# Performance work log

Measured on AMD Instinct MI355X. Metric: run time of the kernel, lower is better.

The kernel has to match this reference:

```python
import jax, jax.numpy as jnp
import numpy as np

B, C, H, W = 8, 256, 64, 64
HEADS, HID = 8, 64
TMP = HEADS * HID  # 512


def setup_inputs() -> dict:
    key = jax.random.key(0)
    ks = jax.random.split(key, 6)
    s = lambda fan: 1.0 / np.sqrt(fan)
    fmap = jax.random.normal(ks[0], (B, C, H, W), jnp.float32)
    Wq = jax.random.normal(ks[1], (TMP, C), jnp.float32) * s(C)          # to_q 1x1 conv (no bias)
    Wdw = jax.random.normal(ks[2], (C, 1, 3, 3), jnp.float32) * s(9)     # depthwise 3x3 (groups=C, no bias)
    Wkv = jax.random.normal(ks[3], (2 * TMP, C), jnp.float32) * s(C)     # 1x1 conv producing k,v (no bias)
    Wout = jax.random.normal(ks[4], (C, TMP), jnp.float32) * s(TMP)      # to_out 1x1 conv
    bout = jax.random.normal(ks[5], (C,), jnp.float32) * 0.01
    return {"fmap": fmap, "Wq": Wq, "Wdw": Wdw, "Wkv": Wkv, "Wout": Wout, "bout": bout}


def reference(fmap, Wq, Wdw, Wkv, Wout, bout):
    heads, hid = HEADS, HID
    scale = hid ** (-0.5)
    b, c, h, w = fmap.shape
    n = h * w

    # 1x1 conv == channel GEMM
    q = jnp.einsum('bcxy,oc->boxy', fmap, Wq)
    # depthwise 3x3, padding=1
    dw = jax.lax.conv_general_dilated(
        fmap, Wdw, window_strides=(1, 1), padding='SAME',
        dimension_numbers=('NCHW', 'OIHW', 'NCHW'), feature_group_count=c)
    kv = jnp.einsum('bcxy,oc->boxy', dw, Wkv)
    k, v = jnp.split(kv, 2, axis=1)

    # 'b (h c) x y -> b h (x y) c'
    def to_seq(t):
        return t.reshape(b, heads, hid, n).transpose(0, 1, 3, 2)  # [b, h, n, d]

    q, k, v = to_seq(q), to_seq(k), to_seq(v)
    q = jax.nn.softmax(q, axis=-1) * scale   # softmax over feature dim
    k = jax.nn.softmax(k, axis=-2)           # softmax over token dim

    ctx = jnp.einsum('bhnd,bhne->bhde', k, v)    # [b, h, d, d]
    out = jnp.einsum('bhnd,bhde->bhne', q, ctx)  # [b, h, n, d]

    # '(b h) (x y) d -> b (h d) x y'
    out = out.transpose(0, 1, 3, 2).reshape(b, heads * hid, h, w)

    # to_out: GELU (exact) then 1x1 conv with bias (mode='ac')
    out = jax.nn.gelu(out, approximate=False)
    return jnp.einsum('bcxy,oc->boxy', out, Wout) + bout[None, :, None, None]
```

## Files before the change

kernel.cpp:

```cpp
#include <hip/hip_runtime.h>
#include <hip/hip_bf16.h>
#include <math.h>

#define Bx 8
#define Cc 256
#define Nn 4096
#define TMPc 512

typedef unsigned short ushort;
typedef unsigned int uint;
typedef __attribute__((ext_vector_type(8))) short bf16x8;
typedef __attribute__((ext_vector_type(4))) float f32x4;

union F4 { float4 v; float f[4]; };

__device__ __forceinline__ float gelu_exact(float x) {
  return x * 0.5f * (1.0f + erff(x * 0.70710678118654752f));
}
__device__ __forceinline__ ushort f2bf(float x) {
  uint u = __float_as_uint(x);
  uint r = (u + 0x7fffu + ((u >> 16) & 1u)) >> 16;
  return (ushort)r;
}

typedef const __attribute__((address_space(1))) uint* gp1_t;
typedef __attribute__((address_space(3))) uint* lp3_t;
__device__ __forceinline__ void gload16(void* lds, const void* g) {
  __builtin_amdgcn_global_load_lds((gp1_t)g, (lp3_t)lds, 16, 0, 0);
}
__device__ __forceinline__ bf16x8 fragread(const char* lds, int row, int kc) {
  return *(const bf16x8*)(lds + row * 64 + ((kc ^ (row & 3)) << 4));
}

#define CGRP 32
__global__ __launch_bounds__(256) void convfuse_k(const float* __restrict__ fmap,
                                                  const float* __restrict__ Wdw,
                                                  ushort* __restrict__ fmapT,
                                                  ushort* __restrict__ dwT) {
  __shared__ float sin_[CGRP][6 * 64 + 1];
  __shared__ float wl[CGRP][9];
  int t = threadIdx.x;
  int y0 = blockIdx.x * 4;
  int c0 = blockIdx.y * CGRP;
  int z = blockIdx.z;
  for (int i = t; i < CGRP * 9; i += 256) wl[i / 9][i % 9] = Wdw[c0 * 9 + i];
  const float* src = fmap + ((size_t)z * Cc + c0) * 4096;
#pragma unroll
  for (int it = 0; it < 12; ++it) {
    int idx = it * 256 + t;
    int c = idx / 96, rem = idx % 96, yy = rem >> 4, x4 = rem & 15;
    int gy = y0 - 1 + yy;
    F4 v;
    if ((unsigned)gy < 64u)
      v.v = *(const float4*)&src[(size_t)c * 4096 + gy * 64 + x4 * 4];
    else
      v.f[0] = v.f[1] = v.f[2] = v.f[3] = 0.f;
#pragma unroll
    for (int j = 0; j < 4; ++j) sin_[c][yy * 64 + x4 * 4 + j] = v.f[j];
  }
  __syncthreads();
  int c8 = (t & 3) * 8;
  int nl = t >> 2;
  size_t nbase = (size_t)z * 4096 + (size_t)y0 * 64;
#pragma unroll
  for (int it = 0; it < 4; ++it) {
    int n = it * 64 + nl;
    int y = n >> 6, x = n & 63;
    union { ushort u[8]; uint4 q; } fo, go;
#pragma unroll
    for (int cc = 0; cc < 8; ++cc) {
      int c = c8 + cc;
      fo.u[cc] = f2bf(sin_[c][(y + 1) * 64 + x]);
      float acc = 0.f;
#pragma unroll
      for (int dy = 0; dy < 3; ++dy) {
#pragma unroll
        for (int dx = 0; dx < 3; ++dx) {
          int xx = x + dx - 1;
          float pv = ((unsigned)xx < 64u) ? sin_[c][(y + dy) * 64 + xx] : 0.f;
          acc += pv * wl[c][dy * 3 + dx];
        }
      }
      go.u[cc] = f2bf(acc);
    }
    *(uint4*)&fmapT[(nbase + n) * Cc + c0 + c8] = fo.q;
    *(uint4*)&dwT[(nbase + n) * Cc + c0 + c8] = go.q;
  }
}

__global__ __launch_bounds__(256) void cvtb3_k(const float* __restrict__ Wq,
                                               const float* __restrict__ Wkv,
                                               const float* __restrict__ Wout,
                                               ushort* __restrict__ WqB,
                                               ushort* __restrict__ WkvB,
                                               ushort* __restrict__ WoutB) {
  int i = blockIdx.x * 256 + threadIdx.x;
  const float* s;
  ushort* d;
  int idx;
  if (i < 32768) { s = Wq; d = WqB; idx = i; }
  else if (i < 98304) { s = Wkv; d = WkvB; idx = i - 32768; }
  else { s = Wout; d = WoutB; idx = i - 98304; }
  F4 v; v.v = *(const float4*)&s[(size_t)idx * 4];
  union { ushort u[4]; uint2 q; } o;
#pragma unroll
  for (int j = 0; j < 4; ++j) o.u[j] = f2bf(v.f[j]);
  *(uint2*)&d[(size_t)idx * 4] = o.q;
}

__global__ __launch_bounds__(256) void kvgemm_k(const ushort* __restrict__ P,
                                                const ushort* __restrict__ Q,
                                                ushort* __restrict__ Y,
                                                long qz, long yz) {
  __shared__ __align__(16) char lds[16384];
  char* LP = lds;
  char* LQ = lds + 8192;
  int t = threadIdx.x, w = t >> 6, l = t & 63;
  int z = blockIdx.z;
  const ushort* Pz = P + (size_t)(blockIdx.y * 128) * 256;
  const ushort* Qz = Q + (size_t)z * qz + (size_t)(blockIdx.x * 128) * 256;
  f32x4 acc[4][4];
#pragma unroll
  for (int i = 0; i < 4; ++i)
#pragma unroll
    for (int j = 0; j < 4; ++j) acc[i][j] = (f32x4){0.f, 0.f, 0.f, 0.f};
  int wr = (w >> 1) * 64, wc = (w & 1) * 64;
  int rl = l & 15, kc = l >> 4;
  int srow = (l >> 2) & 15, scol = l & 3;

  for (int k0 = 0; k0 < 256; k0 += 32) {
    __syncthreads();
#pragma unroll
    for (int j = 0; j < 2; ++j) {
      int row = (w * 2 + j) * 16 + srow;
      int g = scol ^ (row & 3);
      int off = __builtin_amdgcn_readfirstlane((w * 2 + j) * 1024);
      gload16(LP + off, Pz + (size_t)row * 256 + k0 + g * 8);
      gload16(LQ + off, Qz + (size_t)row * 256 + k0 + g * 8);
    }
    asm volatile("s_waitcnt vmcnt(0)" ::: "memory");
    __syncthreads();
    bf16x8 a[4], b[4];
#pragma unroll
    for (int i = 0; i < 4; ++i) a[i] = fragread(LP, wr + i * 16 + rl, kc);
#pragma unroll
    for (int i = 0; i < 4; ++i) b[i] = fragread(LQ, wc + i * 16 + rl, kc);
#pragma unroll
    for (int i = 0; i < 4; ++i)
#pragma unroll
      for (int j = 0; j < 4; ++j)
        acc[i][j] = __builtin_amdgcn_mfma_f32_16x16x32_bf16(a[i], b[j], acc[i][j], 0, 0, 0);
  }
  int r0 = blockIdx.y * 128 + wr, c0 = blockIdx.x * 128 + wc;
  ushort* Yz = Y + (size_t)z * yz;
#pragma unroll
  for (int i = 0; i < 4; ++i) {
#pragma unroll
    for (int reg = 0; reg < 4; ++reg) {
      int r = r0 + i * 16 + kc * 4 + reg;
#pragma unroll
      for (int j = 0; j < 4; ++j) {
        int c = c0 + j * 16 + rl;
        float v = acc[i][j][reg];
        Yz[(size_t)r * 4096 + c] = f2bf(r < 512 ? __expf(v) : v);
      }
    }
  }
}

__global__ __launch_bounds__(256) void ctx_mfma(const ushort* __restrict__ kv,
                                                float* __restrict__ ctxf,
                                                float* __restrict__ sf) {
  __shared__ __align__(16) char lds[8192];
  int t = threadIdx.x, w = t >> 6, l = t & 63;
  int s = blockIdx.x;
  int h = blockIdx.y & 7, z = blockIdx.y >> 3;
  const ushort* kb = kv + ((size_t)z * 1024 + h * 64) * 4096;
  const ushort* vb = kv + ((size_t)z * 1024 + 512 + h * 64) * 4096;
  f32x4 acc[2][2];
  f32x4 accs[2];
#pragma unroll
  for (int i = 0; i < 2; ++i) {
    accs[i] = (f32x4){0.f, 0.f, 0.f, 0.f};
#pragma unroll
    for (int j = 0; j < 2; ++j) acc[i][j] = (f32x4){0.f, 0.f, 0.f, 0.f};
  }
  bf16x8 ones;
#pragma unroll
  for (int i = 0; i < 8; ++i) ones[i] = (short)0x3F80;
  int wr = (w >> 1) * 32, wc = (w & 1) * 32;
  int rl = l & 15, kc = l >> 4;
  int srow = (l >> 2) & 15, scol = l & 3;
  for (int it = 0; it < 32; ++it) {
    int k0 = s * 1024 + it * 32;
    __syncthreads();
    {
      int row = w * 16 + srow;
      int g = scol ^ (row & 3);
      int off = __builtin_amdgcn_readfirstlane(w * 1024);
      gload16(lds + off, vb + (size_t)row * 4096 + k0 + g * 8);
      gload16(lds + 4096 + off, kb + (size_t)row * 4096 + k0 + g * 8);
    }
    asm volatile("s_waitcnt vmcnt(0)" ::: "memory");
    __syncthreads();
    bf16x8 a[2], b[2];
#pragma unroll
    for (int i = 0; i < 2; ++i) a[i] = fragread(lds, wr + i * 16 + rl, kc);
#pragma unroll
    for (int i = 0; i < 2; ++i) b[i] = fragread(lds + 4096, wc + i * 16 + rl, kc);
#pragma unroll
    for (int i = 0; i < 2; ++i)
#pragma unroll
      for (int j = 0; j < 2; ++j)
        acc[i][j] = __builtin_amdgcn_mfma_f32_16x16x32_bf16(a[i], b[j], acc[i][j], 0, 0, 0);
    if (w < 2) {
#pragma unroll
      for (int j = 0; j < 2; ++j)
        accs[j] = __builtin_amdgcn_mfma_f32_16x16x32_bf16(b[j], ones, accs[j], 0, 0, 0);
    }
  }
  float* cf = ctxf + (size_t)(z * 8 + h) * 4096;
#pragma unroll
  for (int i = 0; i < 2; ++i)
#pragma unroll
    for (int reg = 0; reg < 4; ++reg) {
      int e = wr + i * 16 + kc * 4 + reg;
#pragma unroll
      for (int j = 0; j < 2; ++j) {
        int d = wc + j * 16 + rl;
        atomicAdd(&cf[e * 64 + d], acc[i][j][reg]);
      }
    }
  if (w < 2 && rl == 0) {
    float* sp = sf + (size_t)(z * 8 + h) * 64;
#pragma unroll
    for (int j = 0; j < 2; ++j)
#pragma unroll
      for (int reg = 0; reg < 4; ++reg)
        atomicAdd(&sp[wc + j * 16 + kc * 4 + reg], accs[j][reg]);
  }
}

__global__ __launch_bounds__(256) void ctx_cvt(const float* __restrict__ ctxf,
                                               const float* __restrict__ sf,
                                               ushort* __restrict__ cswz) {
  int page = blockIdx.x;
  const float* s = ctxf + (size_t)page * 4096;
  const float* sp = sf + (size_t)page * 64;
  char* d = (char*)(cswz + (size_t)page * 4096);
  int t = threadIdx.x;
  int e = t >> 2, d0 = (t & 3) * 16;
#pragma unroll
  for (int j = 0; j < 16; ++j) {
    int dd = d0 + j;
    int byte = e * 128 + (((dd >> 3) ^ (e & 7)) << 4) + (dd & 7) * 2;
    *(ushort*)(d + byte) = f2bf(s[e * 64 + dd] / sp[dd]);
  }
}

__global__ __launch_bounds__(256, 2) void qao_k(const ushort* __restrict__ fmapT,
                                                const ushort* __restrict__ WqB,
                                                const ushort* __restrict__ cswz,
                                                const ushort* __restrict__ WoutB,
                                                const float* __restrict__ bout,
                                                float* __restrict__ out) {
  __shared__ __align__(16) char lds[65536];
  char* qbuf = lds;
  char* Bres = lds + 16384;
  char* Asg  = lds + 49152;
  int t = threadIdx.x, w = t >> 6, l = t & 63;
  int z = blockIdx.y, n0 = blockIdx.x * 64;
  int rl = l & 15, kc = l >> 4;
  int srow = (l >> 2) & 15, scol = l & 3;
  int wrd = (w >> 1) * 64;
  int wcn = (w & 1) * 32;
  int hh = w >> 1;

  const ushort* fT = fmapT + ((size_t)z * 4096 + n0) * 256;

#pragma unroll
  for (int p = 0; p < 8; ++p) {
    int row = (w * 8 + p) * 2 + (l >> 5);
    int cs = l & 31;
    int off = __builtin_amdgcn_readfirstlane((w * 8 + p) * 1024);
    gload16(Bres + off, fT + (size_t)row * 256 + ((cs ^ (row & 7)) * 8));
  }

  f32x4 oacc[4][4];
#pragma unroll
  for (int i = 0; i < 4; ++i)
#pragma unroll
    for (int j = 0; j < 4; ++j) oacc[i][j] = (f32x4){0.f, 0.f, 0.f, 0.f};

  asm volatile("s_waitcnt vmcnt(0)" ::: "memory");
  __syncthreads();

  for (int c = 0; c < 4; ++c) {
    const ushort* Wqc = WqB + (size_t)(c * 128) * 256;
    f32x4 qa[4][2];
#pragma unroll
    for (int i = 0; i < 4; ++i)
#pragma unroll
      for (int j = 0; j < 2; ++j) qa[i][j] = (f32x4){0.f, 0.f, 0.f, 0.f};
#pragma unroll
    for (int j = 0; j < 2; ++j) {
      int row = (w * 2 + j) * 16 + srow;
      int g = scol ^ (row & 3);
      int off = __builtin_amdgcn_readfirstlane((w * 2 + j) * 1024);
      gload16(Asg + off, Wqc + (size_t)row * 256 + g * 8);
    }
    asm volatile("s_waitcnt vmcnt(0)" ::: "memory");
    __syncthreads();
#pragma unroll
    for (int k0 = 0; k0 < 256; k0 += 32) {
      char* cur = Asg + (((k0 >> 5) & 1) ? 8192 : 0);
      if (k0 + 32 < 256) {
        char* nxt = Asg + (((k0 >> 5) & 1) ? 0 : 8192);
#pragma unroll
        for (int j = 0; j < 2; ++j) {
          int row = (w * 2 + j) * 16 + srow;
          int g = scol ^ (row & 3);
          int off = __builtin_amdgcn_readfirstlane((w * 2 + j) * 1024);
          gload16(nxt + off, Wqc + (size_t)row * 256 + (k0 + 32) + g * 8);
        }
      }
      bf16x8 a[4], b[2];
#pragma unroll
      for (int i = 0; i < 4; ++i) a[i] = fragread(cur, wrd + i * 16 + rl, kc);
      int g0 = k0 >> 3;
#pragma unroll
      for (int j = 0; j < 2; ++j) {
        int n = wcn + 16 * j + rl;
        b[j] = *(const bf16x8*)(Bres + n * 512 + (((g0 + kc) ^ (n & 7)) << 4));
      }
#pragma unroll
      for (int i = 0; i < 4; ++i)
#pragma unroll
        for (int j = 0; j < 2; ++j)
          qa[i][j] = __builtin_amdgcn_mfma_f32_16x16x32_bf16(a[i], b[j], qa[i][j], 0, 0, 0);
      asm volatile("s_waitcnt vmcnt(0)" ::: "memory");
      __syncthreads();
    }
    {
      const char* cp = (const char*)cswz + (size_t)(z * 8 + c * 2) * 8192;
#pragma unroll
      for (int r = 0; r < 4; ++r) {
        int off = __builtin_amdgcn_readfirstlane(w * 4096 + r * 1024);
        gload16(Asg + off, cp + off + l * 16);
      }
    }
#pragma unroll
    for (int j = 0; j < 2; ++j) {
      float m = -1e30f;
#pragma unroll
      for (int i = 0; i < 4; ++i)
#pragma unroll
        for (int r = 0; r < 4; ++r) m = fmaxf(m, qa[i][j][r]);
      m = fmaxf(m, __shfl_xor(m, 16, 64));
      m = fmaxf(m, __shfl_xor(m, 32, 64));
      float s = 0.f;
#pragma unroll
      for (int i = 0; i < 4; ++i)
#pragma unroll
        for (int r = 0; r < 4; ++r) {
          float e = __expf(qa[i][j][r] - m);
          qa[i][j][r] = e;
          s += e;
        }
      s += __shfl_xor(s, 16, 64);
      s += __shfl_xor(s, 32, 64);
      float inv = 0.125f / s;
#pragma unroll
      for (int i = 0; i < 4; ++i)
#pragma unroll
        for (int r = 0; r < 4; ++r) qa[i][j][r] *= inv;
    }
#pragma unroll
    for (int i = 0; i < 4; ++i)
#pragma unroll
      for (int j = 0; j < 2; ++j) {
        int n = wcn + 16 * j + rl;
        int dby = (wrd + 16 * i + 4 * kc) * 2;
        union { ushort u[4]; unsigned long long q; } pk;
#pragma unroll
        for (int r = 0; r < 4; ++r) pk.u[r] = f2bf(qa[i][j][r]);
        *(unsigned long long*)(qbuf + n * 256 + (dby ^ ((n & 7) << 4))) = pk.q;
      }
    asm volatile("s_waitcnt vmcnt(0)" ::: "memory");
    __syncthreads();
    f32x4 pacc[4][2];
#pragma unroll
    for (int i = 0; i < 4; ++i)
#pragma unroll
      for (int j = 0; j < 2; ++j) pacc[i][j] = (f32x4){0.f, 0.f, 0.f, 0.f};
    const char* ctxpg = Asg + hh * 8192;
#pragma unroll
    for (int s = 0; s < 2; ++s) {
      bf16x8 a[4], b[2];
#pragma unroll
      for (int i = 0; i < 4; ++i) {
        int e = 16 * i + rl;
        a[i] = *(const bf16x8*)(ctxpg + e * 128 + (((s * 4 + kc) ^ (e & 7)) << 4));
      }
#pragma unroll
      for (int j = 0; j < 2; ++j) {
        int n = wcn + 16 * j + rl;
        int dby = hh * 128 + s * 64 + kc * 16;
        b[j] = *(const bf16x8*)(qbuf + n * 256 + (dby ^ ((n & 7) << 4)));
      }
#pragma unroll
      for (int i = 0; i < 4; ++i)
#pragma unroll
        for (int j = 0; j < 2; ++j)
          pacc[i][j] = __builtin_amdgcn_mfma_f32_16x16x32_bf16(a[i], b[j], pacc[i][j], 0, 0, 0);
    }
    __syncthreads();
#pragma unroll
    for (int i = 0; i < 4; ++i)
#pragma unroll
      for (int j = 0; j < 2; ++j) {
        int n = wcn + 16 * j + rl;
        int mby = (hh * 64 + 16 * i + 4 * kc) * 2;
        union { ushort u[4]; unsigned long long q; } pk;
#pragma unroll
        for (int r = 0; r < 4; ++r) pk.u[r] = f2bf(gelu_exact(pacc[i][j][r]));
        *(unsigned long long*)(qbuf + n * 256 + (mby ^ ((n & 7) << 4))) = pk.q;
      }
    __syncthreads();
#pragma unroll
    for (int ks = 0; ks < 4; ++ks) {
      if (ks) __syncthreads();
#pragma unroll
      for (int jj = 0; jj < 4; ++jj) {
        int row = w * 64 + jj * 16 + srow;
        int g = scol ^ (row & 3);
        int off = __builtin_amdgcn_readfirstlane((w * 4 + jj) * 1024);
        gload16(Asg + off, WoutB + (size_t)row * 512 + c * 128 + ks * 32 + g * 8);
      }
      asm volatile("s_waitcnt vmcnt(0)" ::: "memory");
      __syncthreads();
      bf16x8 a[4], b[4];
#pragma unroll
      for (int i = 0; i < 4; ++i) a[i] = fragread(Asg, w * 64 + 16 * i + rl, kc);
#pragma unroll
      for (int j = 0; j < 4; ++j) {
        int n = 16 * j + rl;
        b[j] = *(const bf16x8*)(qbuf + n * 256 + ((ks * 64 + kc * 16) ^ ((n & 7) << 4)));
      }
#pragma unroll
      for (int i = 0; i < 4; ++i)
#pragma unroll
        for (int j = 0; j < 4; ++j)
          oacc[i][j] = __builtin_amdgcn_mfma_f32_16x16x32_bf16(a[i], b[j], oacc[i][j], 0, 0, 0);
    }
    __syncthreads();
  }
  float* oz = out + (size_t)z * Cc * Nn + n0;
#pragma unroll
  for (int i = 0; i < 4; ++i) {
#pragma unroll
    for (int r = 0; r < 4; ++r) {
      int crow = w * 64 + 16 * i + 4 * kc + r;
      float bv = bout[crow];
      float* rowp = oz + (size_t)crow * 4096;
#pragma unroll
      for (int j = 0; j < 4; ++j) rowp[16 * j + rl] = oacc[i][j][r] + bv;
    }
  }
}

extern "C" void kernel_launch(void* const* d_in, const int* in_sizes, int n_in,
                              void* d_out, int out_size, void* d_ws, size_t ws_size,
                              hipStream_t stream) {
  (void)in_sizes; (void)n_in; (void)out_size; (void)ws_size;
  const float* fmap = (const float*)d_in[0];
  const float* Wq   = (const float*)d_in[1];
  const float* Wdw  = (const float*)d_in[2];
  const float* Wkv  = (const float*)d_in[3];
  const float* Wout = (const float*)d_in[4];
  const float* bout = (const float*)d_in[5];
  float* out = (float*)d_out;

  ushort* WqB   = (ushort*)d_ws;
  ushort* WkvB  = WqB + 512 * 256;
  ushort* WoutB = WkvB + 1024 * 256;
  ushort* fmapT = WoutB + 256 * 512;
  ushort* dwT   = fmapT + (size_t)Bx * 4096 * 256;
  ushort* kv    = dwT + (size_t)Bx * 4096 * 256;
  ushort* cswz  = kv + (size_t)Bx * 1024 * 4096;
  float*  ctxf  = (float*)(cswz + (size_t)Bx * 8 * 4096);
  float*  sf    = ctxf + (size_t)Bx * 8 * 64 * 64;

  cvtb3_k<<<dim3(512), 256, 0, stream>>>(Wq, Wkv, Wout, WqB, WkvB, WoutB);
  convfuse_k<<<dim3(16, Cc / CGRP, Bx), 256, 0, stream>>>(fmap, Wdw, fmapT, dwT);
  kvgemm_k<<<dim3(32, 8, Bx), 256, 0, stream>>>(
      WkvB, dwT, kv, (long)4096 * 256, (long)1024 * 4096);
  hipMemsetAsync(ctxf, 0, (size_t)Bx * 8 * (4096 + 64) * sizeof(float), stream);
  ctx_mfma<<<dim3(4, Bx * 8), 256, 0, stream>>>(kv, ctxf, sf);
  ctx_cvt<<<dim3(Bx * 8), 256, 0, stream>>>(ctxf, sf, cswz);
  qao_k<<<dim3(64, Bx), 256, 0, stream>>>(fmapT, WqB, cswz, WoutB, bout, out);
}
```

Measured before the change: 127.3 us.

## Load Wq, Wout and context fragments directly from global into registers, dropping LDS staging

The fused q/attention/out kernel no longer stages Wq, the context matrix and Wout tiles through LDS. Each wave now reads its MFMA A-fragments straight from global memory, relying on cache reuse across blocks. This removes many barriers and the 16KB staging area, so LDS drops to 48KB and launch bounds rise to 3 blocks per CU. ctx_cvt now writes an unswizzled row-major bf16 context with vectorised stores. The cost is exposed global-load latency per MFMA step with no software prefetch, plus possible register pressure from holding the context fragments.

```diff
diff --git a/kernel.cpp b/kernel.cpp
--- a/kernel.cpp
+++ b/kernel.cpp
@@ -243,35 +243,35 @@
 
 __global__ __launch_bounds__(256) void ctx_cvt(const float* __restrict__ ctxf,
                                                const float* __restrict__ sf,
-                                               ushort* __restrict__ cswz) {
+                                               ushort* __restrict__ ctxb) {
   int page = blockIdx.x;
   const float* s = ctxf + (size_t)page * 4096;
   const float* sp = sf + (size_t)page * 64;
-  char* d = (char*)(cswz + (size_t)page * 4096);
+  ushort* d = ctxb + (size_t)page * 4096;
   int t = threadIdx.x;
   int e = t >> 2, d0 = (t & 3) * 16;
+  union { ushort u[16]; uint4 q[2]; } o;
 #pragma unroll
   for (int j = 0; j < 16; ++j) {
     int dd = d0 + j;
-    int byte = e * 128 + (((dd >> 3) ^ (e & 7)) << 4) + (dd & 7) * 2;
-    *(ushort*)(d + byte) = f2bf(s[e * 64 + dd] / sp[dd]);
-  }
-}
-
-__global__ __launch_bounds__(256, 2) void qao_k(const ushort* __restrict__ fmapT,
+    o.u[j] = f2bf(s[e * 64 + dd] / sp[dd]);
+  }
+  uint4* dp = (uint4*)&d[e * 64 + d0];
+  dp[0] = o.q[0]; dp[1] = o.q[1];
+}
+
+__global__ __launch_bounds__(256, 3) void qao_k(const ushort* __restrict__ fmapT,
                                                 const ushort* __restrict__ WqB,
-                                                const ushort* __restrict__ cswz,
+                                                const ushort* __restrict__ ctxb,
                                                 const ushort* __restrict__ WoutB,
                                                 const float* __restrict__ bout,
                                                 float* __restrict__ out) {
-  __shared__ __align__(16) char lds[65536];
+  __shared__ __align__(16) char lds[49152];
   char* qbuf = lds;
   char* Bres = lds + 16384;
-  char* Asg  = lds + 49152;
   int t = threadIdx.x, w = t >> 6, l = t & 63;
   int z = blockIdx.y, n0 = blockIdx.x * 64;
   int rl = l & 15, kc = l >> 4;
-  int srow = (l >> 2) & 15, scol = l & 3;
   int wrd = (w >> 1) * 64;
   int wcn = (w & 1) * 32;
   int hh = w >> 1;
@@ -296,37 +296,17 @@
   __syncthreads();
 
   for (int c = 0; c < 4; ++c) {
-    const ushort* Wqc = WqB + (size_t)(c * 128) * 256;
     f32x4 qa[4][2];
 #pragma unroll
     for (int i = 0; i < 4; ++i)
 #pragma unroll
       for (int j = 0; j < 2; ++j) qa[i][j] = (f32x4){0.f, 0.f, 0.f, 0.f};
 #pragma unroll
-    for (int j = 0; j < 2; ++j) {
-      int row = (w * 2 + j) * 16 + srow;
-      int g = scol ^ (row & 3);
-      int off = __builtin_amdgcn_readfirstlane((w * 2 + j) * 1024);
-      gload16(Asg + off, Wqc + (size_t)row * 256 + g * 8);
-    }
-    asm volatile("s_waitcnt vmcnt(0)" ::: "memory");
-    __syncthreads();
-#pragma unroll
     for (int k0 = 0; k0 < 256; k0 += 32) {
-      char* cur = Asg + (((k0 >> 5) & 1) ? 8192 : 0);
-      if (k0 + 32 < 256) {
-        char* nxt = Asg + (((k0 >> 5) & 1) ? 0 : 8192);
-#pragma unroll
-        for (int j = 0; j < 2; ++j) {
-          int row = (w * 2 + j) * 16 + srow;
-          int g = scol ^ (row & 3);
-          int off = __builtin_amdgcn_readfirstlane((w * 2 + j) * 1024);
-          gload16(nxt + off, Wqc + (size_t)row * 256 + (k0 + 32) + g * 8);
-        }
-      }
       bf16x8 a[4], b[2];
 #pragma unroll
-      for (int i = 0; i < 4; ++i) a[i] = fragread(cur, wrd + i * 16 + rl, kc);
+      for (int i = 0; i < 4; ++i)
+        a[i] = *(const bf16x8*)(WqB + (size_t)(c * 128 + wrd + 16 * i + rl) * 256 + k0 + kc * 8);
       int g0 = k0 >> 3;
 #pragma unroll
       for (int j = 0; j < 2; ++j) {
@@ -338,17 +318,14 @@
 #pragma unroll
         for (int j = 0; j < 2; ++j)
           qa[i][j] = __builtin_amdgcn_mfma_f32_16x16x32_bf16(a[i], b[j], qa[i][j], 0, 0, 0);
-      asm volatile("s_waitcnt vmcnt(0)" ::: "memory");
-      __syncthreads();
-    }
-    {
-      const char* cp = (const char*)cswz + (size_t)(z * 8 + c * 2) * 8192;
-#pragma unroll
-      for (int r = 0; r < 4; ++r) {
-        int off = __builtin_amdgcn_readfirstlane(w * 4096 + r * 1024);
-        gload16(Asg + off, cp + off + l * 16);
-      }
-    }
+    }
+    const ushort* cpg = ctxb + (size_t)(z * 8 + c * 2 + hh) * 4096;
+    bf16x8 ca[2][4];
+#pragma unroll
+    for (int s = 0; s < 2; ++s)
+#pragma unroll
+      for (int i = 0; i < 4; ++i)
+        ca[s][i] = *(const bf16x8*)(cpg + (size_t)(16 * i + rl) * 64 + s * 32 + kc * 8);
 #pragma unroll
     for (int j = 0; j < 2; ++j) {
       float m = -1e30f;
@@ -375,6 +352,7 @@
 #pragma unroll
         for (int r = 0; r < 4; ++r) qa[i][j][r] *= inv;
     }
+    __syncthreads();
 #pragma unroll
     for (int i = 0; i < 4; ++i)
 #pragma unroll
@@ -386,41 +364,32 @@
         for (int r = 0; r < 4; ++r) pk.u[r] = f2bf(qa[i][j][r]);
         *(unsigned long long*)(qbuf + n * 256 + (dby ^ ((n & 7) << 4))) = pk.q;
       }
-    asm volatile("s_waitcnt vmcnt(0)" ::: "memory");
-    __syncthreads();
     f32x4 pacc[4][2];
 #pragma unroll
     for (int i = 0; i < 4; ++i)
 #pragma unroll
       for (int j = 0; j < 2; ++j) pacc[i][j] = (f32x4){0.f, 0.f, 0.f, 0.f};
-    const char* ctxpg = Asg + hh * 8192;
 #pragma unroll
     for (int s = 0; s < 2; ++s) {
-      bf16x8 a[4], b[2];
-#pragma unroll
-      for (int i = 0; i < 4; ++i) {
-        int e = 16 * i + rl;
-        a[i] = *(const bf16x8*)(ctxpg + e * 128 + (((s * 4 + kc) ^ (e & 7)) << 4));
-      }
+      bf16x8 b[2];
 #pragma unroll
       for (int j = 0; j < 2; ++j) {
         int n = wcn + 16 * j + rl;
-        int dby = hh * 128 + s * 64 + kc * 16;
+        int dby = wrd * 2 + s * 64 + kc * 16;
         b[j] = *(const bf16x8*)(qbuf + n * 256 + (dby ^ ((n & 7) << 4)));
       }
 #pragma unroll
       for (int i = 0; i < 4; ++i)
 #pragma unroll
         for (int j = 0; j < 2; ++j)
-          pacc[i][j] = __builtin_amdgcn_mfma_f32_16x16x32_bf16(a[i], b[j], pacc[i][j], 0, 0, 0);
-    }
-    __syncthreads();
+          pacc[i][j] = __builtin_amdgcn_mfma_f32_16x16x32_bf16(ca[s][i], b[j], pacc[i][j], 0, 0, 0);
+    }
 #pragma unroll
     for (int i = 0; i < 4; ++i)
 #pragma unroll
       for (int j = 0; j < 2; ++j) {
         int n = wcn + 16 * j + rl;
-        int mby = (hh * 64 + 16 * i + 4 * kc) * 2;
+        int mby = (wrd + 16 * i + 4 * kc) * 2;
         union { ushort u[4]; unsigned long long q; } pk;
 #pragma unroll
         for (int r = 0; r < 4; ++r) pk.u[r] = f2bf(gelu_exact(pacc[i][j][r]));
@@ -429,19 +398,11 @@
     __syncthreads();
 #pragma unroll
     for (int ks = 0; ks < 4; ++ks) {
-      if (ks) __syncthreads();
-#pragma unroll
-      for (int jj = 0; jj < 4; ++jj) {
-        int row = w * 64 + jj * 16 + srow;
-        int g = scol ^ (row & 3);
-        int off = __builtin_amdgcn_readfirstlane((w * 4 + jj) * 1024);
-        gload16(Asg + off, WoutB + (size_t)row * 512 + c * 128 + ks * 32 + g * 8);
-      }
-      asm volatile("s_waitcnt vmcnt(0)" ::: "memory");
-      __syncthreads();
       bf16x8 a[4], b[4];
 #pragma unroll
-      for (int i = 0; i < 4; ++i) a[i] = fragread(Asg, w * 64 + 16 * i + rl, kc);
+      for (int i = 0; i < 4; ++i)
+        a[i] = *(const bf16x8*)(WoutB + (size_t)(w * 64 + 16 * i + rl) * 512 +
+                                c * 128 + ks * 32 + kc * 8);
 #pragma unroll
       for (int j = 0; j < 4; ++j) {
         int n = 16 * j + rl;
@@ -453,7 +414,6 @@
         for (int j = 0; j < 4; ++j)
           oacc[i][j] = __builtin_amdgcn_mfma_f32_16x16x32_bf16(a[i], b[j], oacc[i][j], 0, 0, 0);
     }
-    __syncthreads();
   }
   float* oz = out + (size_t)z * Cc * Nn + n0;
 #pragma unroll
@@ -487,8 +447,8 @@
   ushort* fmapT = WoutB + 256 * 512;
   ushort* dwT   = fmapT + (size_t)Bx * 4096 * 256;
   ushort* kv    = dwT + (size_t)Bx * 4096 * 256;
-  ushort* cswz  = kv + (size_t)Bx * 1024 * 4096;
-  float*  ctxf  = (float*)(cswz + (size_t)Bx * 8 * 4096);
+  ushort* ctxb  = kv + (size_t)Bx * 1024 * 4096;
+  float*  ctxf  = (float*)(ctxb + (size_t)Bx * 8 * 4096);
   float*  sf    = ctxf + (size_t)Bx * 8 * 64 * 64;
 
   cvtb3_k<<<dim3(512), 256, 0, stream>>>(Wq, Wkv, Wout, WqB, WkvB, WoutB);
@@ -497,6 +457,6 @@
       WkvB, dwT, kv, (long)4096 * 256, (long)1024 * 4096);
   hipMemsetAsync(ctxf, 0, (size_t)Bx * 8 * (4096 + 64) * sizeof(float), stream);
   ctx_mfma<<<dim3(4, Bx * 8), 256, 0, stream>>>(kv, ctxf, sf);
-  ctx_cvt<<<dim3(Bx * 8), 256, 0, stream>>>(ctxf, sf, cswz);
-  qao_k<<<dim3(64, Bx), 256, 0, stream>>>(fmapT, WqB, cswz, WoutB, bout, out);
-}
+  ctx_cvt<<<dim3(Bx * 8), 256, 0, stream>>>(ctxf, sf, ctxb);
+  qao_k<<<dim3(64, Bx), 256, 0, stream>>>(fmapT, WqB, ctxb, WoutB, bout, out);
+}
```

Result: slower. 149.9 us (+17.8%).

## Keep dwT tile resident in LDS and stream Wkv chunks with double buffering

Applied to the files above, without the earlier changes.

Rewrites the kv GEMM so each block loads a 64-token x 256-channel slice of dwT into LDS once and loops over eight 128-row chunks of Wkv. Wkv k-slices are double-buffered so the next slice loads while MFMAs run on the current one. This removes repeated reloading of the activation operand across output-row blocks. The cost is a larger LDS footprint (48KB, launch bounds of 2 blocks per CU) and fewer, longer blocks. Separately, ctx_mfma now splits the token dimension into 8 slices instead of 4 to launch more blocks.

```diff
diff --git a/kernel.cpp b/kernel.cpp
--- a/kernel.cpp
+++ b/kernel.cpp
@@ -108,61 +108,87 @@
   *(uint2*)&d[(size_t)idx * 4] = o.q;
 }
 
-__global__ __launch_bounds__(256) void kvgemm_k(const ushort* __restrict__ P,
-                                                const ushort* __restrict__ Q,
-                                                ushort* __restrict__ Y,
-                                                long qz, long yz) {
-  __shared__ __align__(16) char lds[16384];
-  char* LP = lds;
-  char* LQ = lds + 8192;
+__global__ __launch_bounds__(256, 2) void kvgemm2_k(const ushort* __restrict__ WkvB,
+                                                    const ushort* __restrict__ dwT,
+                                                    ushort* __restrict__ kv) {
+  __shared__ __align__(16) char lds[49152];
+  char* Bres = lds;
+  char* Asg  = lds + 32768;
   int t = threadIdx.x, w = t >> 6, l = t & 63;
-  int z = blockIdx.z;
-  const ushort* Pz = P + (size_t)(blockIdx.y * 128) * 256;
-  const ushort* Qz = Q + (size_t)z * qz + (size_t)(blockIdx.x * 128) * 256;
-  f32x4 acc[4][4];
-#pragma unroll
-  for (int i = 0; i < 4; ++i)
-#pragma unroll
-    for (int j = 0; j < 4; ++j) acc[i][j] = (f32x4){0.f, 0.f, 0.f, 0.f};
-  int wr = (w >> 1) * 64, wc = (w & 1) * 64;
+  int z = blockIdx.y, n0 = blockIdx.x * 64;
   int rl = l & 15, kc = l >> 4;
   int srow = (l >> 2) & 15, scol = l & 3;
-
-  for (int k0 = 0; k0 < 256; k0 += 32) {
-    __syncthreads();
+  int wr = (w >> 1) * 64, wc = (w & 1) * 32;
+
+  const ushort* dT = dwT + ((size_t)z * 4096 + n0) * 256;
+#pragma unroll
+  for (int p = 0; p < 8; ++p) {
+    int row = (w * 8 + p) * 2 + (l >> 5);
+    int cs = l & 31;
+    int off = __builtin_amdgcn_readfirstlane((w * 8 + p) * 1024);
+    gload16(Bres + off, dT + (size_t)row * 256 + ((cs ^ (row & 7)) * 8));
+  }
+  asm volatile("s_waitcnt vmcnt(0)" ::: "memory");
+  __syncthreads();
+
+  ushort* kz = kv + (size_t)z * 1024 * 4096;
+  for (int c = 0; c < 8; ++c) {
+    const ushort* Wc = WkvB + (size_t)(c * 128) * 256;
+    f32x4 acc[4][2];
+#pragma unroll
+    for (int i = 0; i < 4; ++i)
+#pragma unroll
+      for (int j = 0; j < 2; ++j) acc[i][j] = (f32x4){0.f, 0.f, 0.f, 0.f};
 #pragma unroll
     for (int j = 0; j < 2; ++j) {
       int row = (w * 2 + j) * 16 + srow;
       int g = scol ^ (row & 3);
       int off = __builtin_amdgcn_readfirstlane((w * 2 + j) * 1024);
-      gload16(LP + off, Pz + (size_t)row * 256 + k0 + g * 8);
-      gload16(LQ + off, Qz + (size_t)row * 256 + k0 + g * 8);
+      gload16(Asg + off, Wc + (size_t)row * 256 + g * 8);
     }
     asm volatile("s_waitcnt vmcnt(0)" ::: "memory");
     __syncthreads();
-    bf16x8 a[4], b[4];
-#pragma unroll
-    for (int i = 0; i < 4; ++i) a[i] = fragread(LP, wr + i * 16 + rl, kc);
-#pragma unroll
-    for (int i = 0; i < 4; ++i) b[i] = fragread(LQ, wc + i * 16 + rl, kc);
-#pragma unroll
-    for (int i = 0; i < 4; ++i)
-#pragma unroll
-      for (int j = 0; j < 4; ++j)
-        acc[i][j] = __builtin_amdgcn_mfma_f32_16x16x32_bf16(a[i], b[j], acc[i][j], 0, 0, 0);
-  }
-  int r0 = blockIdx.y * 128 + wr, c0 = blockIdx.x * 128 + wc;
-  ushort* Yz = Y + (size_t)z * yz;
-#pragma unroll
-  for (int i = 0; i < 4; ++i) {
-#pragma unroll
-    for (int reg = 0; reg < 4; ++reg) {
-      int r = r0 + i * 16 + kc * 4 + reg;
-#pragma unroll
-      for (int j = 0; j < 4; ++j) {
-        int c = c0 + j * 16 + rl;
-        float v = acc[i][j][reg];
-        Yz[(size_t)r * 4096 + c] = f2bf(r < 512 ? __expf(v) : v);
+#pragma unroll
+    for (int k0 = 0; k0 < 256; k0 += 32) {
+      char* cur = Asg + (((k0 >> 5) & 1) ? 8192 : 0);
+      if (k0 + 32 < 256) {
+        char* nxt = Asg + (((k0 >> 5) & 1) ? 0 : 8192);
+#pragma unroll
+        for (int j = 0; j < 2; ++j) {
+          int row = (w * 2 + j) * 16 + srow;
+          int g = scol ^ (row & 3);
+          int off = __builtin_amdgcn_readfirstlane((w * 2 + j) * 1024);
+          gload16(nxt + off, Wc + (size_t)row * 256 + (k0 + 32) + g * 8);
+        }
+      }
+      bf16x8 a[4], b[2];
+#pragma unroll
+      for (int i = 0; i < 4; ++i) a[i] = fragread(cur, wr + i * 16 + rl, kc);
+      int g0 = k0 >> 3;
+#pragma unroll
+      for (int j = 0; j < 2; ++j) {
+        int n = wc + 16 * j + rl;
+        b[j] = *(const bf16x8*)(Bres + n * 512 + (((g0 + kc) ^ (n & 7)) << 4));
+      }
+#pragma unroll
+      for (int i = 0; i < 4; ++i)
+#pragma unroll
+        for (int j = 0; j < 2; ++j)
+          acc[i][j] = __builtin_amdgcn_mfma_f32_16x16x32_bf16(a[i], b[j], acc[i][j], 0, 0, 0);
+      asm volatile("s_waitcnt vmcnt(0)" ::: "memory");
+      __syncthreads();
+    }
+#pragma unroll
+    for (int i = 0; i < 4; ++i) {
+#pragma unroll
+      for (int reg = 0; reg < 4; ++reg) {
+        int r = c * 128 + wr + i * 16 + kc * 4 + reg;
+#pragma unroll
+        for (int j = 0; j < 2; ++j) {
+          int col = n0 + wc + j * 16 + rl;
+          float v = acc[i][j][reg];
+          kz[(size_t)r * 4096 + col] = f2bf(c < 4 ? __expf(v) : v);
+        }
       }
     }
   }
@@ -191,8 +217,8 @@
   int wr = (w >> 1) * 32, wc = (w & 1) * 32;
   int rl = l & 15, kc = l >> 4;
   int srow = (l >> 2) & 15, scol = l & 3;
-  for (int it = 0; it < 32; ++it) {
-    int k0 = s * 1024 + it * 32;
+  for (int it = 0; it < 16; ++it) {
+    int k0 = s * 512 + it * 32;
     __syncthreads();
     {
       int row = w * 16 + srow;
@@ -493,10 +519,9 @@
 
   cvtb3_k<<<dim3(512), 256, 0, stream>>>(Wq, Wkv, Wout, WqB, WkvB, WoutB);
   convfuse_k<<<dim3(16, Cc / CGRP, Bx), 256, 0, stream>>>(fmap, Wdw, fmapT, dwT);
-  kvgemm_k<<<dim3(32, 8, Bx), 256, 0, stream>>>(
-      WkvB, dwT, kv, (long)4096 * 256, (long)1024 * 4096);
+  kvgemm2_k<<<dim3(64, Bx), 256, 0, stream>>>(WkvB, dwT, kv);
   hipMemsetAsync(ctxf, 0, (size_t)Bx * 8 * (4096 + 64) * sizeof(float), stream);
-  ctx_mfma<<<dim3(4, Bx * 8), 256, 0, stream>>>(kv, ctxf, sf);
+  ctx_mfma<<<dim3(8, Bx * 8), 256, 0, stream>>>(kv, ctxf, sf);
   ctx_cvt<<<dim3(Bx * 8), 256, 0, stream>>>(ctxf, sf, cswz);
   qao_k<<<dim3(64, Bx), 256, 0, stream>>>(fmapT, WqB, cswz, WoutB, bout, out);
 }
```

Result: slower. 131.2 us (+3.0%).
